# Kernel optimization log

Measured on AMD Instinct MI355X. Metric: run time of the kernel, lower is better.

Reference implementation:

```python
import jax, jax.numpy as jnp
import numpy as np

N_NODES = 50000
N_EDGES = 50000  # hyperedges
NNZ = 500000
N_GRAPHS = 50
IN_C, HID, OUT_C = 128, 256, 2


def _inv_deg(idx, num_segments):
    deg = jax.ops.segment_sum(jnp.ones(idx.shape[0], jnp.float32), idx, num_segments=num_segments)
    return jnp.where(deg > 0, 1.0 / deg, 0.0)


def hg_conv(x, W, b, rows, cols, dinv, binv):
    # PyG HypergraphConv (no attention, unit edge weights):
    # X' = D^{-1} H B^{-1} H^T (X Theta) + bias
    x = x @ W                                                    # [N, hid]
    e = jax.ops.segment_sum(x[rows], cols, num_segments=N_EDGES) * binv[:, None]   # edge feats [E, hid]
    out = jax.ops.segment_sum(e[cols], rows, num_segments=N_NODES) * dinv[:, None]  # node feats [N, hid]
    return out + b


def setup_inputs() -> dict:
    key = jax.random.key(0)
    ks = jax.random.split(key, 12)
    x = jax.random.normal(ks[0], (N_NODES, IN_C), jnp.float32)
    edge_index = jax.random.randint(ks[1], (2, NNZ), 0, N_EDGES, dtype=jnp.int64)
    batch = jnp.sort(jax.random.randint(ks[2], (N_NODES,), 0, N_GRAPHS, dtype=jnp.int64))
    s = 0.05
    return {
        "x": x, "edge_index": edge_index, "batch": batch,
        "W0": jax.random.normal(ks[3], (IN_C, HID), jnp.float32) * s,
        "b0": jnp.zeros((HID,), jnp.float32),
        "W1": jax.random.normal(ks[4], (HID, HID), jnp.float32) * s,
        "b1": jnp.zeros((HID,), jnp.float32),
        "W2": jax.random.normal(ks[5], (HID, HID), jnp.float32) * s,
        "b2": jnp.zeros((HID,), jnp.float32),
        "M1": jax.random.normal(ks[6], (HID, HID), jnp.float32) * s,
        "bM1": jnp.zeros((HID,), jnp.float32),
        "M2": jax.random.normal(ks[7], (HID, OUT_C), jnp.float32) * s,
        "bM2": jnp.zeros((OUT_C,), jnp.float32),
    }


def reference(x, edge_index, batch, W0, b0, W1, b1, W2, b2, M1, bM1, M2, bM2):
    rows, cols = edge_index[0], edge_index[1]
    dinv = _inv_deg(rows, N_NODES)   # node degree inverse
    binv = _inv_deg(cols, N_EDGES)   # hyperedge degree inverse
    h = jax.nn.relu(hg_conv(x, W0, b0, rows, cols, dinv, binv))
    h = jax.nn.relu(hg_conv(h, W1, b1, rows, cols, dinv, binv))
    h = jax.nn.relu(hg_conv(h, W2, b2, rows, cols, dinv, binv))
    # global_mean_pool (dropout is identity in eval mode)
    cnt = jax.ops.segment_sum(jnp.ones(N_NODES, jnp.float32), batch, num_segments=N_GRAPHS)
    pooled = jax.ops.segment_sum(h, batch, num_segments=N_GRAPHS) / jnp.maximum(cnt, 1.0)[:, None]
    # MLP head
    out = jax.nn.relu(pooled @ M1 + bM1) @ M2 + bM2
    return out
```

## Files before the change

kernel.cpp:

```cpp
#include <hip/hip_runtime.h>
#include <hip/hip_bf16.h>

#define NN   50000
#define NE   50000
#define NNZV 500000
#define NG   50
#define INC  128
#define HID  256
#define OUTC 2
#define STRIDE 32

typedef __bf16 bf16_t;
typedef __bf16 bf16x8 __attribute__((ext_vector_type(8)));
typedef float  f32x4  __attribute__((ext_vector_type(4)));
typedef float  f32x2  __attribute__((ext_vector_type(2)));

__device__ __forceinline__ bf16_t f2b(float f) {
  union { __hip_bfloat16 h; bf16_t b; } u;
  u.h = __float2bfloat16(f);
  return u.b;
}
__device__ __forceinline__ float b2f(bf16_t b) { return (float)b; }

template <bool HI>
__device__ __forceinline__ unsigned int fp8_pk2(float a, float b, unsigned int old) {
  return __builtin_amdgcn_cvt_pk_fp8_f32(a, b, old, HI);
}
__device__ __forceinline__ uint4 fp8_pk16(const float* v) {
  uint4 o;
  unsigned int* ow = &o.x;
#pragma unroll
  for (int wd = 0; wd < 4; wd++) {
    unsigned int u = fp8_pk2<false>(v[wd * 4 + 0], v[wd * 4 + 1], 0u);
    ow[wd] = fp8_pk2<true>(v[wd * 4 + 2], v[wd * 4 + 3], u);
  }
  return o;
}
__device__ __forceinline__ void fp8_acc16(uint4 v, f32x2* a2) {
  a2[0] += __builtin_amdgcn_cvt_pk_f32_fp8(v.x, false);
  a2[1] += __builtin_amdgcn_cvt_pk_f32_fp8(v.x, true);
  a2[2] += __builtin_amdgcn_cvt_pk_f32_fp8(v.y, false);
  a2[3] += __builtin_amdgcn_cvt_pk_f32_fp8(v.y, true);
  a2[4] += __builtin_amdgcn_cvt_pk_f32_fp8(v.z, false);
  a2[5] += __builtin_amdgcn_cvt_pk_f32_fp8(v.z, true);
  a2[6] += __builtin_amdgcn_cvt_pk_f32_fp8(v.w, false);
  a2[7] += __builtin_amdgcn_cvt_pk_f32_fp8(v.w, true);
}

__device__ __forceinline__ void wswiz_one(const float* __restrict__ W, bf16_t* __restrict__ wsw, int t) {
  int lane = t & 63;
  int nt   = (t >> 6) & 15;
  int kc   = t >> 10;
  int q = lane >> 4, n16 = lane & 15;
  bf16x8 o;
#pragma unroll
  for (int j = 0; j < 8; j++)
    o[j] = f2b(W[(size_t)(kc * 32 + q * 8 + j) * HID + nt * 16 + n16]);
  reinterpret_cast<bf16x8*>(wsw)[t] = o;
}

#define FILL_EPT   4
#define FILL_CHUNK (256 * FILL_EPT)
#define FILL_B     ((NNZV + FILL_CHUNK - 1) / FILL_CHUNK)
#define PREP_BX 1563
#define PREP_BW 80
#define PREP_BG 196

__global__ void build_kernel(const int* __restrict__ rows, const int* __restrict__ cols,
                             int* __restrict__ ncur, int* __restrict__ ecur,
                             unsigned short* __restrict__ ncol, unsigned short* __restrict__ erow,
                             const float* __restrict__ x, unsigned char* __restrict__ xb8,
                             const float* __restrict__ W0, const float* __restrict__ W1,
                             const float* __restrict__ W2, bf16_t* __restrict__ w0,
                             bf16_t* __restrict__ w1, bf16_t* __restrict__ w2,
                             const int* __restrict__ batch, int* __restrict__ gstart) {
  int blk = blockIdx.x;
  if (blk < FILL_B) {
    int base = blk * FILL_CHUNK + threadIdx.x;
#pragma unroll
    for (int e = 0; e < FILL_EPT; e++) {
      int i = base + e * 256;
      if (i < NNZV) {
        int r = rows[i], c = cols[i];
        int pe = atomicAdd(&ecur[c], 1);
        if (pe < STRIDE) erow[((size_t)c << 5) + pe] = (unsigned short)r;
        int pn = atomicAdd(&ncur[r], 1);
        if (pn < STRIDE) ncol[((size_t)r << 5) + pn] = (unsigned short)c;
      }
    }
  } else if (blk < FILL_B + PREP_BX) {
    int t = (blk - FILL_B) * 256 + threadIdx.x;
    if (t >= NN * INC / 16) return;
    const f32x4* p = reinterpret_cast<const f32x4*>(x) + (size_t)t * 4;
    float v[16];
#pragma unroll
    for (int wd = 0; wd < 4; wd++) {
      f32x4 q4 = p[wd];
#pragma unroll
      for (int j = 0; j < 4; j++) v[wd * 4 + j] = q4[j];
    }
    reinterpret_cast<uint4*>(xb8)[t] = fp8_pk16(v);
  } else if (blk < FILL_B + PREP_BX + PREP_BW) {
    int t = (blk - FILL_B - PREP_BX) * 256 + threadIdx.x;
    const int C0 = (INC / 32) * 1024;
    const int C1 = (HID / 32) * 1024;
    if (t < C0)                wswiz_one(W0, w0, t);
    else if (t < C0 + C1)      wswiz_one(W1, w1, t - C0);
    else if (t < C0 + 2 * C1)  wswiz_one(W2, w2, t - C0 - C1);
  } else {
    int i = (blk - FILL_B - PREP_BX - PREP_BW) * 256 + threadIdx.x;
    if (i >= NN) return;
    int cur  = batch[i];
    int prev = (i == 0) ? -1 : batch[i - 1];
    for (int g = prev + 1; g <= cur; g++) gstart[g] = i;
    if (i == NN - 1) {
      for (int g = cur + 1; g <= NG; g++) gstart[g] = NN;
    }
  }
}

template <int K>
__device__ __forceinline__ void gather_seg(const unsigned char* __restrict__ src,
                                           const int* __restrict__ cnt,
                                           const unsigned short* __restrict__ lst,
                                           int seg, int grp, int lr, float* acc, int& c) {
  constexpr int LPR  = K / 16;
  constexpr int NPAR = 64 / LPR;
  constexpr int MAXE = STRIDE / NPAR;
  c = min(cnt[seg], STRIDE);
  int jbeg = (c * grp) / NPAR;
  int jend = (c * (grp + 1)) / NPAR;
  int n    = jend - jbeg;
  const unsigned short* p = lst + ((size_t)seg << 5) + jbeg;
  const uint4* sv = reinterpret_cast<const uint4*>(src);
  uint4 v[MAXE];
#pragma unroll
  for (int i = 0; i < MAXE; i++) {
    if (i < n) v[i] = sv[(size_t)p[i] * LPR + lr];
  }
  f32x2* a2 = reinterpret_cast<f32x2*>(acc);
#pragma unroll
  for (int k = 0; k < 8; k++) a2[k] = f32x2{0.f, 0.f};
#pragma unroll
  for (int i = 0; i < MAXE; i++) {
    if (i < n) fp8_acc16(v[i], a2);
  }
#pragma unroll
  for (int mask = LPR; mask < 64; mask <<= 1) {
#pragma unroll
    for (int k = 0; k < 16; k++) acc[k] += __shfl_xor(acc[k], mask, 64);
  }
}

template <int W>
__global__ void seg_gather_kernel(const unsigned char* __restrict__ src,
                                  const int* __restrict__ cnt,
                                  const unsigned short* __restrict__ lst,
                                  unsigned char* __restrict__ dst, int nseg) {
  constexpr int LPR = W / 16;
  int seg  = blockIdx.x * 4 + (threadIdx.x >> 6);
  int lane = threadIdx.x & 63;
  if (seg >= nseg) return;
  int grp = lane / LPR, lr = lane % LPR;
  float acc[16];
  int c;
  gather_seg<W>(src, cnt, lst, seg, grp, lr, acc, c);
  if (grp == 0) {
    float sc = (c > 0) ? (1.0f / (float)c) : 0.f;
    float v16[16];
#pragma unroll
    for (int k = 0; k < 16; k++) v16[k] = acc[k] * sc;
    reinterpret_cast<uint4*>(dst + (size_t)seg * W + lr * 16)[0] = fp8_pk16(v16);
  }
}

template <int K, bool GRELU, bool EPI, bool OUT8>
__global__ __launch_bounds__(256) void ngemm_kernel(const unsigned char* __restrict__ src,
                                                    const int* __restrict__ cnt,
                                                    const unsigned short* __restrict__ lst,
                                                    const float* __restrict__ gbias,
                                                    const bf16_t* __restrict__ wsw,
                                                    const float* __restrict__ ebias,
                                                    void* __restrict__ Bout, int M) {
  constexpr int SW = K + 8;
  __shared__ bf16_t arows[16 * SW];
  const int tid  = threadIdx.x;
  const int wid  = tid >> 6;
  const int lane = tid & 63;
  const int mblk = blockIdx.x * 16;

  constexpr int LPR = K / 16;
  int grp = lane / LPR, lr = lane % LPR;
#pragma unroll
  for (int i = 0; i < 4; i++) {
    int row = wid * 4 + i;
    int seg = mblk + row;
    if (seg < M) {
      float acc[16];
      int c;
      gather_seg<K>(src, cnt, lst, seg, grp, lr, acc, c);
      if (grp == 0) {
        float sc = (c > 0) ? (1.0f / (float)c) : 0.f;
        bf16_t* dp = arows + row * SW + lr * 16;
        bf16x8 o0, o1;
#pragma unroll
        for (int k = 0; k < 8; k++) {
          float v0 = acc[k] * sc, v1 = acc[k + 8] * sc;
          if constexpr (GRELU) {
            v0 = fmaxf(v0 + gbias[lr * 16 + k], 0.f);
            v1 = fmaxf(v1 + gbias[lr * 16 + k + 8], 0.f);
          }
          o0[k] = f2b(v0);
          o1[k] = f2b(v1);
        }
        reinterpret_cast<bf16x8*>(dp)[0] = o0;
        reinterpret_cast<bf16x8*>(dp)[1] = o1;
      }
    }
  }
  __syncthreads();

  const int q = lane >> 4, n16 = lane & 15;
  f32x4 acc2[4];
#pragma unroll
  for (int j = 0; j < 4; j++) acc2[j] = f32x4{0.f, 0.f, 0.f, 0.f};

  const bf16x8* wv = reinterpret_cast<const bf16x8*>(wsw);
  for (int kc = 0; kc < K / 32; kc++) {
    bf16x8 af = *reinterpret_cast<const bf16x8*>(arows + n16 * SW + kc * 32 + q * 8);
    const bf16x8* wp = wv + (size_t)kc * 1024 + (size_t)(wid * 4) * 64 + lane;
#pragma unroll
    for (int j = 0; j < 4; j++) {
      bf16x8 bf = wp[j * 64];
      acc2[j] = __builtin_amdgcn_mfma_f32_16x16x32_bf16(af, bf, acc2[j], 0, 0, 0);
    }
  }

  float bcol[4];
  if constexpr (EPI) {
#pragma unroll
    for (int j = 0; j < 4; j++) bcol[j] = ebias[(wid * 4 + j) * 16 + n16];
  }

  int mb = mblk + q * 4;
#pragma unroll
  for (int r = 0; r < 4; r++) {
    int m = mb + r;
    if (m < M) {
      if constexpr (OUT8) {
        unsigned char* dst = (unsigned char*)Bout + (size_t)m * HID + n16;
#pragma unroll
        for (int j = 0; j < 4; j++) {
          float v = acc2[j][r];
          if constexpr (EPI) v = fmaxf(v + bcol[j], 0.f);
          unsigned int wbits = fp8_pk2<false>(v, v, 0u);
          dst[(wid * 4 + j) << 4] = (unsigned char)(wbits & 0xffu);
        }
      } else {
        bf16_t* dst = (bf16_t*)Bout + (size_t)m * HID + n16;
#pragma unroll
        for (int j = 0; j < 4; j++) {
          float v = acc2[j][r];
          if constexpr (EPI) v = fmaxf(v + bcol[j], 0.f);
          dst[(wid * 4 + j) << 4] = f2b(v);
        }
      }
    }
  }
}

template <int K>
__global__ __launch_bounds__(256) void ngemm2_kernel(const unsigned char* __restrict__ src,
                                                     const int* __restrict__ cnt,
                                                     const unsigned short* __restrict__ lst,
                                                     const bf16_t* __restrict__ wswA,
                                                     const float* __restrict__ biasA,
                                                     const bf16_t* __restrict__ wswB,
                                                     unsigned char* __restrict__ Bout, int M) {
  constexpr int SW  = K + 8;
  constexpr int SW2 = HID + 8;
  __shared__ bf16_t arows[16 * SW];
  __shared__ bf16_t brows[16 * SW2];
  const int tid  = threadIdx.x;
  const int wid  = tid >> 6;
  const int lane = tid & 63;
  const int mblk = blockIdx.x * 16;

  constexpr int LPR = K / 16;
  int grp = lane / LPR, lr = lane % LPR;
#pragma unroll
  for (int i = 0; i < 4; i++) {
    int row = wid * 4 + i;
    int seg = mblk + row;
    if (seg < M) {
      float acc[16];
      int c;
      gather_seg<K>(src, cnt, lst, seg, grp, lr, acc, c);
      if (grp == 0) {
        float sc = (c > 0) ? (1.0f / (float)c) : 0.f;
        bf16_t* dp = arows + row * SW + lr * 16;
        bf16x8 o0, o1;
#pragma unroll
        for (int k = 0; k < 8; k++) {
          o0[k] = f2b(acc[k] * sc);
          o1[k] = f2b(acc[k + 8] * sc);
        }
        reinterpret_cast<bf16x8*>(dp)[0] = o0;
        reinterpret_cast<bf16x8*>(dp)[1] = o1;
      }
    }
  }
  __syncthreads();

  const int q = lane >> 4, n16 = lane & 15;
  {
    f32x4 acc2[4];
#pragma unroll
    for (int j = 0; j < 4; j++) acc2[j] = f32x4{0.f, 0.f, 0.f, 0.f};
    const bf16x8* wv = reinterpret_cast<const bf16x8*>(wswA);
    for (int kc = 0; kc < K / 32; kc++) {
      bf16x8 af = *reinterpret_cast<const bf16x8*>(arows + n16 * SW + kc * 32 + q * 8);
      const bf16x8* wp = wv + (size_t)kc * 1024 + (size_t)(wid * 4) * 64 + lane;
#pragma unroll
      for (int j = 0; j < 4; j++) {
        bf16x8 bf = wp[j * 64];
        acc2[j] = __builtin_amdgcn_mfma_f32_16x16x32_bf16(af, bf, acc2[j], 0, 0, 0);
      }
    }
#pragma unroll
    for (int j = 0; j < 4; j++) {
      float bj = biasA[(wid * 4 + j) * 16 + n16];
#pragma unroll
      for (int r = 0; r < 4; r++) {
        float v = fmaxf(acc2[j][r] + bj, 0.f);
        brows[(q * 4 + r) * SW2 + (wid * 4 + j) * 16 + n16] = f2b(v);
      }
    }
  }
  __syncthreads();

  f32x4 acc3[4];
#pragma unroll
  for (int j = 0; j < 4; j++) acc3[j] = f32x4{0.f, 0.f, 0.f, 0.f};
  const bf16x8* wv = reinterpret_cast<const bf16x8*>(wswB);
  for (int kc = 0; kc < HID / 32; kc++) {
    bf16x8 af = *reinterpret_cast<const bf16x8*>(brows + n16 * SW2 + kc * 32 + q * 8);
    const bf16x8* wp = wv + (size_t)kc * 1024 + (size_t)(wid * 4) * 64 + lane;
#pragma unroll
    for (int j = 0; j < 4; j++) {
      bf16x8 bf = wp[j * 64];
      acc3[j] = __builtin_amdgcn_mfma_f32_16x16x32_bf16(af, bf, acc3[j], 0, 0, 0);
    }
  }

  int mb = mblk + q * 4;
#pragma unroll
  for (int r = 0; r < 4; r++) {
    int m = mb + r;
    if (m < M) {
      unsigned char* dst = Bout + (size_t)m * HID + n16;
#pragma unroll
      for (int j = 0; j < 4; j++) {
        float v = acc3[j][r];
        unsigned int wbits = fp8_pk2<false>(v, v, 0u);
        dst[(wid * 4 + j) << 4] = (unsigned char)(wbits & 0xffu);
      }
    }
  }
}

__global__ __launch_bounds__(256) void npool_kernel(const unsigned char* __restrict__ src,
                                                    const int* __restrict__ cnt,
                                                    const unsigned short* __restrict__ lst,
                                                    const float* __restrict__ bias,
                                                    const int* __restrict__ batch,
                                                    float* __restrict__ pooled) {
  constexpr int K = HID, SW = K + 8;
  __shared__ bf16_t arows[16 * SW];
  const int tid  = threadIdx.x;
  const int wid  = tid >> 6;
  const int lane = tid & 63;
  const int mblk = blockIdx.x * 16;

  constexpr int LPR = K / 16;
  int grp = lane / LPR, lr = lane % LPR;
#pragma unroll
  for (int i = 0; i < 4; i++) {
    int row = wid * 4 + i;
    int seg = mblk + row;
    if (seg < NN) {
      float acc[16];
      int c;
      gather_seg<K>(src, cnt, lst, seg, grp, lr, acc, c);
      if (grp == 0) {
        float sc = (c > 0) ? (1.0f / (float)c) : 0.f;
        bf16_t* dp = arows + row * SW + lr * 16;
        bf16x8 o0, o1;
#pragma unroll
        for (int k = 0; k < 8; k++) {
          o0[k] = f2b(fmaxf(acc[k] * sc + bias[lr * 16 + k], 0.f));
          o1[k] = f2b(fmaxf(acc[k + 8] * sc + bias[lr * 16 + k + 8], 0.f));
        }
        reinterpret_cast<bf16x8*>(dp)[0] = o0;
        reinterpret_cast<bf16x8*>(dp)[1] = o1;
      }
    }
  }
  __syncthreads();

  int f = tid;
  float acc = 0.f;
  int curg = -1;
  for (int r = 0; r < 16; r++) {
    int node = mblk + r;
    if (node >= NN) break;
    int g = batch[node];
    if (g != curg) {
      if (curg >= 0) atomicAdd(&pooled[(size_t)curg * HID + f], acc);
      curg = g; acc = 0.f;
    }
    acc += b2f(arows[r * SW + f]);
  }
  if (curg >= 0) atomicAdd(&pooled[(size_t)curg * HID + f], acc);
}

__global__ void head_kernel(const float* __restrict__ pooled, const int* __restrict__ gstart,
                            const float* __restrict__ M1, const float* __restrict__ bM1,
                            const float* __restrict__ M2, const float* __restrict__ bM2,
                            float* __restrict__ out) {
  int g = blockIdx.x;
  int t = threadIdx.x;
  __shared__ float p[HID];
  __shared__ float red[256];
  float cntf = (float)(gstart[g + 1] - gstart[g]);
  float inv = 1.f / fmaxf(cntf, 1.f);
  p[t] = pooled[(size_t)g * HID + t] * inv;
  __syncthreads();
  float h = bM1[t];
  for (int k = 0; k < HID; k++) h += p[k] * M1[k * HID + t];
  h = fmaxf(h, 0.f);
  float c0 = h * M2[t * OUTC + 0];
  float c1 = h * M2[t * OUTC + 1];
  red[t] = c0;
  __syncthreads();
  for (int off = 128; off > 0; off >>= 1) {
    if (t < off) red[t] += red[t + off];
    __syncthreads();
  }
  float s0 = 0.f;
  if (t == 0) s0 = red[0];
  __syncthreads();
  red[t] = c1;
  __syncthreads();
  for (int off = 128; off > 0; off >>= 1) {
    if (t < off) red[t] += red[t + off];
    __syncthreads();
  }
  if (t == 0) {
    out[g * 2 + 0] = s0 + bM2[0];
    out[g * 2 + 1] = red[0] + bM2[1];
  }
}

extern "C" void kernel_launch(void* const* d_in, const int* in_sizes, int n_in,
                              void* d_out, int out_size, void* d_ws, size_t ws_size,
                              hipStream_t stream) {
  const float* x   = (const float*)d_in[0];
  const int* ei    = (const int*)d_in[1];
  const int* rows  = ei;
  const int* cols  = ei + NNZV;
  const int* batch = (const int*)d_in[2];
  const float* W0  = (const float*)d_in[3];
  const float* b0  = (const float*)d_in[4];
  const float* W1  = (const float*)d_in[5];
  const float* b1  = (const float*)d_in[6];
  const float* W2  = (const float*)d_in[7];
  const float* b2  = (const float*)d_in[8];
  const float* M1  = (const float*)d_in[9];
  const float* bM1 = (const float*)d_in[10];
  const float* M2  = (const float*)d_in[11];
  const float* bM2 = (const float*)d_in[12];
  float* out       = (float*)d_out;

  char* w = (char*)d_ws;
  size_t off = 0;
  bf16_t* P = (bf16_t*)(w + off); off += (size_t)NN * HID * 2;
  bf16_t* Q = (bf16_t*)(w + off); off += (size_t)NE * HID * 2;
  bf16_t* R = (bf16_t*)(w + off); off += (size_t)NN * HID * 2;
  bf16_t* wsw0 = (bf16_t*)(w + off); off += (size_t)INC * HID * 2;
  bf16_t* wsw1 = (bf16_t*)(w + off); off += (size_t)HID * HID * 2;
  bf16_t* wsw2 = (bf16_t*)(w + off); off += (size_t)HID * HID * 2;
  int* gstart   = (int*)(w + off);   off += (size_t)(NG + 1) * 4;
  size_t zoff = off;
  float* pooled = (float*)(w + off); off += (size_t)NG * HID * 4;
  int* ncur     = (int*)(w + off);   off += (size_t)NN * 4;
  int* ecur     = (int*)(w + off);   off += (size_t)NE * 4;
  size_t zbytes = off - zoff;
  off = (off + 63) & ~(size_t)63;
  unsigned short* erow = (unsigned short*)(w + off); off += (size_t)NE * STRIDE * 2;
  unsigned short* ncol = (unsigned short*)(w + off); off += (size_t)NN * STRIDE * 2;

  unsigned char* xb8 = (unsigned char*)R;
  unsigned char* Qe8 = (unsigned char*)Q;
  unsigned char* Q8  = (unsigned char*)Q;
  unsigned char* P8  = (unsigned char*)P;

  (void)hipMemsetAsync(w + zoff, 0, zbytes, stream);

  const int BN = 256;
  build_kernel<<<FILL_B + PREP_BX + PREP_BW + PREP_BG, BN, 0, stream>>>(
      rows, cols, ncur, ecur, ncol, erow, x, xb8, W0, W1, W2, wsw0, wsw1, wsw2, batch, gstart);

  const int ROW_GRID16 = (NN + 15) / 16;
  const int SEG_GRID  = (NN + 3) / 4;

  seg_gather_kernel<INC><<<SEG_GRID, BN, 0, stream>>>(xb8, ecur, erow, Qe8, NE);
  ngemm2_kernel<INC><<<ROW_GRID16, BN, 0, stream>>>(Qe8, ncur, ncol, wsw0, b0, wsw1, P8, NN);
  seg_gather_kernel<HID><<<SEG_GRID, BN, 0, stream>>>(P8, ecur, erow, Q8, NE);
  ngemm_kernel<HID, true, false, true><<<ROW_GRID16, BN, 0, stream>>>(
      Q8, ncur, ncol, b1, wsw2, nullptr, P8, NN);
  seg_gather_kernel<HID><<<SEG_GRID, BN, 0, stream>>>(P8, ecur, erow, Q8, NE);
  npool_kernel<<<ROW_GRID16, BN, 0, stream>>>(Q8, ncur, ncol, b2, batch, pooled);

  head_kernel<<<NG, 256, 0, stream>>>(pooled, gstart, M1, bM1, M2, bM2, out);
}
```

Baseline: 376.4 us.

## Assign one segment per lane group and drop cross-lane shuffle reductions in gathers

The gather path changes. Instead of spreading one segment's neighbour list across every lane group of a wave and combining the partial sums with xor-shuffle reductions, each lane group now owns a whole segment and walks its list in chunks of 8. This removes the 16-way shuffle reduction and the idle lanes on the store, and packs more segments into each block. The grids are resized to match, and ngemm2 now processes 32 rows per block with two MFMA row tiles so the weight loads are reused. The fill loop is also simplified to one edge per thread. In exchange, per-lane work now depends on each segment's degree, which can cause load imbalance within a wave, and memory-level parallelism per segment is lower.

```diff
diff --git a/kernel.cpp b/kernel.cpp
--- a/kernel.cpp
+++ b/kernel.cpp
@@ -59,9 +59,7 @@
   reinterpret_cast<bf16x8*>(wsw)[t] = o;
 }
 
-#define FILL_EPT   4
-#define FILL_CHUNK (256 * FILL_EPT)
-#define FILL_B     ((NNZV + FILL_CHUNK - 1) / FILL_CHUNK)
+#define FILL_B ((NNZV + 255) / 256)
 #define PREP_BX 1563
 #define PREP_BW 80
 #define PREP_BG 196
@@ -76,17 +74,13 @@
                              const int* __restrict__ batch, int* __restrict__ gstart) {
   int blk = blockIdx.x;
   if (blk < FILL_B) {
-    int base = blk * FILL_CHUNK + threadIdx.x;
-#pragma unroll
-    for (int e = 0; e < FILL_EPT; e++) {
-      int i = base + e * 256;
-      if (i < NNZV) {
-        int r = rows[i], c = cols[i];
-        int pe = atomicAdd(&ecur[c], 1);
-        if (pe < STRIDE) erow[((size_t)c << 5) + pe] = (unsigned short)r;
-        int pn = atomicAdd(&ncur[r], 1);
-        if (pn < STRIDE) ncol[((size_t)r << 5) + pn] = (unsigned short)c;
-      }
+    int i = blk * 256 + threadIdx.x;
+    if (i < NNZV) {
+      int r = rows[i], c = cols[i];
+      int pe = atomicAdd(&ecur[c], 1);
+      int pn = atomicAdd(&ncur[r], 1);
+      if (pe < STRIDE) erow[((size_t)c << 5) + pe] = (unsigned short)r;
+      if (pn < STRIDE) ncol[((size_t)r << 5) + pn] = (unsigned short)c;
     }
   } else if (blk < FILL_B + PREP_BX) {
     int t = (blk - FILL_B) * 256 + threadIdx.x;
@@ -120,58 +114,50 @@
 }
 
 template <int K>
-__device__ __forceinline__ void gather_seg(const unsigned char* __restrict__ src,
-                                           const int* __restrict__ cnt,
-                                           const unsigned short* __restrict__ lst,
-                                           int seg, int grp, int lr, float* acc, int& c) {
-  constexpr int LPR  = K / 16;
-  constexpr int NPAR = 64 / LPR;
-  constexpr int MAXE = STRIDE / NPAR;
+__device__ __forceinline__ void gather_direct(const unsigned char* __restrict__ src,
+                                              const int* __restrict__ cnt,
+                                              const unsigned short* __restrict__ lst,
+                                              int seg, int lr, float* acc, int& c) {
+  constexpr int LPR = K / 16;
   c = min(cnt[seg], STRIDE);
-  int jbeg = (c * grp) / NPAR;
-  int jend = (c * (grp + 1)) / NPAR;
-  int n    = jend - jbeg;
-  const unsigned short* p = lst + ((size_t)seg << 5) + jbeg;
+  const unsigned short* p = lst + ((size_t)seg << 5);
   const uint4* sv = reinterpret_cast<const uint4*>(src);
-  uint4 v[MAXE];
-#pragma unroll
-  for (int i = 0; i < MAXE; i++) {
-    if (i < n) v[i] = sv[(size_t)p[i] * LPR + lr];
-  }
   f32x2* a2 = reinterpret_cast<f32x2*>(acc);
 #pragma unroll
   for (int k = 0; k < 8; k++) a2[k] = f32x2{0.f, 0.f};
-#pragma unroll
-  for (int i = 0; i < MAXE; i++) {
-    if (i < n) fp8_acc16(v[i], a2);
-  }
-#pragma unroll
-  for (int mask = LPR; mask < 64; mask <<= 1) {
-#pragma unroll
-    for (int k = 0; k < 16; k++) acc[k] += __shfl_xor(acc[k], mask, 64);
+  for (int i0 = 0; i0 < c; i0 += 8) {
+    int m = c - i0;
+    uint4 v[8];
+#pragma unroll
+    for (int j = 0; j < 8; j++)
+      if (j < m) v[j] = sv[(size_t)p[i0 + j] * LPR + lr];
+#pragma unroll
+    for (int j = 0; j < 8; j++)
+      if (j < m) fp8_acc16(v[j], a2);
   }
 }
 
 template <int W>
-__global__ void seg_gather_kernel(const unsigned char* __restrict__ src,
-                                  const int* __restrict__ cnt,
-                                  const unsigned short* __restrict__ lst,
-                                  unsigned char* __restrict__ dst, int nseg) {
+__global__ __launch_bounds__(256) void seg_gather_kernel(const unsigned char* __restrict__ src,
+                                                         const int* __restrict__ cnt,
+                                                         const unsigned short* __restrict__ lst,
+                                                         unsigned char* __restrict__ dst, int nseg) {
   constexpr int LPR = W / 16;
-  int seg  = blockIdx.x * 4 + (threadIdx.x >> 6);
-  int lane = threadIdx.x & 63;
+  constexpr int SPW = 64 / LPR;
+  constexpr int SPB = 4 * SPW;
+  const int lane = threadIdx.x & 63;
+  const int wid  = threadIdx.x >> 6;
+  const int sub  = lane / LPR, lr = lane % LPR;
+  int seg = blockIdx.x * SPB + wid * SPW + sub;
   if (seg >= nseg) return;
-  int grp = lane / LPR, lr = lane % LPR;
   float acc[16];
   int c;
-  gather_seg<W>(src, cnt, lst, seg, grp, lr, acc, c);
-  if (grp == 0) {
-    float sc = (c > 0) ? (1.0f / (float)c) : 0.f;
-    float v16[16];
-#pragma unroll
-    for (int k = 0; k < 16; k++) v16[k] = acc[k] * sc;
-    reinterpret_cast<uint4*>(dst + (size_t)seg * W + lr * 16)[0] = fp8_pk16(v16);
-  }
+  gather_direct<W>(src, cnt, lst, seg, lr, acc, c);
+  float sc = (c > 0) ? (1.0f / (float)c) : 0.f;
+  float v16[16];
+#pragma unroll
+  for (int k = 0; k < 16; k++) v16[k] = acc[k] * sc;
+  reinterpret_cast<uint4*>(dst + (size_t)seg * W + lr * 16)[0] = fp8_pk16(v16);
 }
 
 template <int K, bool GRELU, bool EPI, bool OUT8>
@@ -190,32 +176,30 @@
   const int mblk = blockIdx.x * 16;
 
   constexpr int LPR = K / 16;
-  int grp = lane / LPR, lr = lane % LPR;
-#pragma unroll
-  for (int i = 0; i < 4; i++) {
-    int row = wid * 4 + i;
+  constexpr int SPW = 64 / LPR;
+  const int sub = lane / LPR, lr = lane % LPR;
+  {
+    int row = wid * SPW + sub;
     int seg = mblk + row;
     if (seg < M) {
       float acc[16];
       int c;
-      gather_seg<K>(src, cnt, lst, seg, grp, lr, acc, c);
-      if (grp == 0) {
-        float sc = (c > 0) ? (1.0f / (float)c) : 0.f;
-        bf16_t* dp = arows + row * SW + lr * 16;
-        bf16x8 o0, o1;
-#pragma unroll
-        for (int k = 0; k < 8; k++) {
-          float v0 = acc[k] * sc, v1 = acc[k + 8] * sc;
-          if constexpr (GRELU) {
-            v0 = fmaxf(v0 + gbias[lr * 16 + k], 0.f);
-            v1 = fmaxf(v1 + gbias[lr * 16 + k + 8], 0.f);
-          }
-          o0[k] = f2b(v0);
-          o1[k] = f2b(v1);
+      gather_direct<K>(src, cnt, lst, seg, lr, acc, c);
+      float sc = (c > 0) ? (1.0f / (float)c) : 0.f;
+      bf16_t* dp = arows + row * SW + lr * 16;
+      bf16x8 o0, o1;
+#pragma unroll
+      for (int k = 0; k < 8; k++) {
+        float v0 = acc[k] * sc, v1 = acc[k + 8] * sc;
+        if constexpr (GRELU) {
+          v0 = fmaxf(v0 + gbias[lr * 16 + k], 0.f);
+          v1 = fmaxf(v1 + gbias[lr * 16 + k + 8], 0.f);
         }
-        reinterpret_cast<bf16x8*>(dp)[0] = o0;
-        reinterpret_cast<bf16x8*>(dp)[1] = o1;
-      }
+        o0[k] = f2b(v0);
+        o1[k] = f2b(v1);
+      }
+      reinterpret_cast<bf16x8*>(dp)[0] = o0;
+      reinterpret_cast<bf16x8*>(dp)[1] = o1;
     }
   }
   __syncthreads();
@@ -279,91 +263,103 @@
                                                      unsigned char* __restrict__ Bout, int M) {
   constexpr int SW  = K + 8;
   constexpr int SW2 = HID + 8;
-  __shared__ bf16_t arows[16 * SW];
-  __shared__ bf16_t brows[16 * SW2];
+  constexpr int LPR = K / 16;
+  constexpr int SPW = 64 / LPR;
+  __shared__ bf16_t arows[32 * SW];
+  __shared__ bf16_t brows[32 * SW2];
   const int tid  = threadIdx.x;
   const int wid  = tid >> 6;
   const int lane = tid & 63;
-  const int mblk = blockIdx.x * 16;
-
-  constexpr int LPR = K / 16;
-  int grp = lane / LPR, lr = lane % LPR;
-#pragma unroll
-  for (int i = 0; i < 4; i++) {
-    int row = wid * 4 + i;
+  const int mblk = blockIdx.x * 32;
+
+  {
+    const int sub = lane / LPR, lr = lane % LPR;
+    int row = wid * SPW + sub;
     int seg = mblk + row;
     if (seg < M) {
       float acc[16];
       int c;
-      gather_seg<K>(src, cnt, lst, seg, grp, lr, acc, c);
-      if (grp == 0) {
-        float sc = (c > 0) ? (1.0f / (float)c) : 0.f;
-        bf16_t* dp = arows + row * SW + lr * 16;
-        bf16x8 o0, o1;
-#pragma unroll
-        for (int k = 0; k < 8; k++) {
-          o0[k] = f2b(acc[k] * sc);
-          o1[k] = f2b(acc[k + 8] * sc);
-        }
-        reinterpret_cast<bf16x8*>(dp)[0] = o0;
-        reinterpret_cast<bf16x8*>(dp)[1] = o1;
-      }
+      gather_direct<K>(src, cnt, lst, seg, lr, acc, c);
+      float sc = (c > 0) ? (1.0f / (float)c) : 0.f;
+      bf16_t* dp = arows + row * SW + lr * 16;
+      bf16x8 o0, o1;
+#pragma unroll
+      for (int k = 0; k < 8; k++) {
+        o0[k] = f2b(acc[k] * sc);
+        o1[k] = f2b(acc[k + 8] * sc);
+      }
+      reinterpret_cast<bf16x8*>(dp)[0] = o0;
+      reinterpret_cast<bf16x8*>(dp)[1] = o1;
     }
   }
   __syncthreads();
 
   const int q = lane >> 4, n16 = lane & 15;
   {
-    f32x4 acc2[4];
-#pragma unroll
-    for (int j = 0; j < 4; j++) acc2[j] = f32x4{0.f, 0.f, 0.f, 0.f};
+    f32x4 acc2[2][4];
+#pragma unroll
+    for (int a = 0; a < 2; a++)
+#pragma unroll
+      for (int j = 0; j < 4; j++) acc2[a][j] = f32x4{0.f, 0.f, 0.f, 0.f};
     const bf16x8* wv = reinterpret_cast<const bf16x8*>(wswA);
     for (int kc = 0; kc < K / 32; kc++) {
-      bf16x8 af = *reinterpret_cast<const bf16x8*>(arows + n16 * SW + kc * 32 + q * 8);
+      bf16x8 af0 = *reinterpret_cast<const bf16x8*>(arows + n16 * SW + kc * 32 + q * 8);
+      bf16x8 af1 = *reinterpret_cast<const bf16x8*>(arows + (n16 + 16) * SW + kc * 32 + q * 8);
       const bf16x8* wp = wv + (size_t)kc * 1024 + (size_t)(wid * 4) * 64 + lane;
 #pragma unroll
       for (int j = 0; j < 4; j++) {
         bf16x8 bf = wp[j * 64];
-        acc2[j] = __builtin_amdgcn_mfma_f32_16x16x32_bf16(af, bf, acc2[j], 0, 0, 0);
-      }
-    }
-#pragma unroll
-    for (int j = 0; j < 4; j++) {
-      float bj = biasA[(wid * 4 + j) * 16 + n16];
-#pragma unroll
-      for (int r = 0; r < 4; r++) {
-        float v = fmaxf(acc2[j][r] + bj, 0.f);
-        brows[(q * 4 + r) * SW2 + (wid * 4 + j) * 16 + n16] = f2b(v);
-      }
-    }
-  }
-  __syncthreads();
-
-  f32x4 acc3[4];
-#pragma unroll
-  for (int j = 0; j < 4; j++) acc3[j] = f32x4{0.f, 0.f, 0.f, 0.f};
+        acc2[0][j] = __builtin_amdgcn_mfma_f32_16x16x32_bf16(af0, bf, acc2[0][j], 0, 0, 0);
+        acc2[1][j] = __builtin_amdgcn_mfma_f32_16x16x32_bf16(af1, bf, acc2[1][j], 0, 0, 0);
+      }
+    }
+#pragma unroll
+    for (int a = 0; a < 2; a++) {
+#pragma unroll
+      for (int j = 0; j < 4; j++) {
+        float bj = biasA[(wid * 4 + j) * 16 + n16];
+#pragma unroll
+        for (int r = 0; r < 4; r++) {
+          float v = fmaxf(acc2[a][j][r] + bj, 0.f);
+          brows[(a * 16 + q * 4 + r) * SW2 + (wid * 4 + j) * 16 + n16] = f2b(v);
+        }
+      }
+    }
+  }
+  __syncthreads();
+
+  f32x4 acc3[2][4];
+#pragma unroll
+  for (int a = 0; a < 2; a++)
+#pragma unroll
+    for (int j = 0; j < 4; j++) acc3[a][j] = f32x4{0.f, 0.f, 0.f, 0.f};
   const bf16x8* wv = reinterpret_cast<const bf16x8*>(wswB);
   for (int kc = 0; kc < HID / 32; kc++) {
-    bf16x8 af = *reinterpret_cast<const bf16x8*>(brows + n16 * SW2 + kc * 32 + q * 8);
+    bf16x8 af0 = *reinterpret_cast<const bf16x8*>(brows + n16 * SW2 + kc * 32 + q * 8);
+    bf16x8 af1 = *reinterpret_cast<const bf16x8*>(brows + (n16 + 16) * SW2 + kc * 32 + q * 8);
     const bf16x8* wp = wv + (size_t)kc * 1024 + (size_t)(wid * 4) * 64 + lane;
 #pragma unroll
     for (int j = 0; j < 4; j++) {
       bf16x8 bf = wp[j * 64];
-      acc3[j] = __builtin_amdgcn_mfma_f32_16x16x32_bf16(af, bf, acc3[j], 0, 0, 0);
-    }
-  }
-
-  int mb = mblk + q * 4;
-#pragma unroll
-  for (int r = 0; r < 4; r++) {
-    int m = mb + r;
-    if (m < M) {
-      unsigned char* dst = Bout + (size_t)m * HID + n16;
-#pragma unroll
-      for (int j = 0; j < 4; j++) {
-        float v = acc3[j][r];
-        unsigned int wbits = fp8_pk2<false>(v, v, 0u);
-        dst[(wid * 4 + j) << 4] = (unsigned char)(wbits & 0xffu);
+      acc3[0][j] = __builtin_amdgcn_mfma_f32_16x16x32_bf16(af0, bf, acc3[0][j], 0, 0, 0);
+      acc3[1][j] = __builtin_amdgcn_mfma_f32_16x16x32_bf16(af1, bf, acc3[1][j], 0, 0, 0);
+    }
+  }
+
+#pragma unroll
+  for (int a = 0; a < 2; a++) {
+    int mb = mblk + a * 16 + q * 4;
+#pragma unroll
+    for (int r = 0; r < 4; r++) {
+      int m = mb + r;
+      if (m < M) {
+        unsigned char* dst = Bout + (size_t)m * HID + n16;
+#pragma unroll
+        for (int j = 0; j < 4; j++) {
+          float v = acc3[a][j][r];
+          unsigned int wbits = fp8_pk2<false>(v, v, 0u);
+          dst[(wid * 4 + j) << 4] = (unsigned char)(wbits & 0xffu);
+        }
       }
     }
   }
@@ -383,27 +379,25 @@
   const int mblk = blockIdx.x * 16;
 
   constexpr int LPR = K / 16;
-  int grp = lane / LPR, lr = lane % LPR;
-#pragma unroll
-  for (int i = 0; i < 4; i++) {
-    int row = wid * 4 + i;
+  constexpr int SPW = 64 / LPR;
+  const int sub = lane / LPR, lr = lane % LPR;
+  {
+    int row = wid * SPW + sub;
     int seg = mblk + row;
     if (seg < NN) {
       float acc[16];
       int c;
-      gather_seg<K>(src, cnt, lst, seg, grp, lr, acc, c);
-      if (grp == 0) {
-        float sc = (c > 0) ? (1.0f / (float)c) : 0.f;
-        bf16_t* dp = arows + row * SW + lr * 16;
-        bf16x8 o0, o1;
-#pragma unroll
-        for (int k = 0; k < 8; k++) {
-          o0[k] = f2b(fmaxf(acc[k] * sc + bias[lr * 16 + k], 0.f));
-          o1[k] = f2b(fmaxf(acc[k + 8] * sc + bias[lr * 16 + k + 8], 0.f));
-        }
-        reinterpret_cast<bf16x8*>(dp)[0] = o0;
-        reinterpret_cast<bf16x8*>(dp)[1] = o1;
-      }
+      gather_direct<K>(src, cnt, lst, seg, lr, acc, c);
+      float sc = (c > 0) ? (1.0f / (float)c) : 0.f;
+      bf16_t* dp = arows + row * SW + lr * 16;
+      bf16x8 o0, o1;
+#pragma unroll
+      for (int k = 0; k < 8; k++) {
+        o0[k] = f2b(fmaxf(acc[k] * sc + bias[lr * 16 + k], 0.f));
+        o1[k] = f2b(fmaxf(acc[k + 8] * sc + bias[lr * 16 + k + 8], 0.f));
+      }
+      reinterpret_cast<bf16x8*>(dp)[0] = o0;
+      reinterpret_cast<bf16x8*>(dp)[1] = o1;
     }
   }
   __syncthreads();
@@ -511,16 +505,13 @@
   build_kernel<<<FILL_B + PREP_BX + PREP_BW + PREP_BG, BN, 0, stream>>>(
       rows, cols, ncur, ecur, ncol, erow, x, xb8, W0, W1, W2, wsw0, wsw1, wsw2, batch, gstart);
 
-  const int ROW_GRID16 = (NN + 15) / 16;
-  const int SEG_GRID  = (NN + 3) / 4;
-
-  seg_gather_kernel<INC><<<SEG_GRID, BN, 0, stream>>>(xb8, ecur, erow, Qe8, NE);
-  ngemm2_kernel<INC><<<ROW_GRID16, BN, 0, stream>>>(Qe8, ncur, ncol, wsw0, b0, wsw1, P8, NN);
-  seg_gather_kernel<HID><<<SEG_GRID, BN, 0, stream>>>(P8, ecur, erow, Q8, NE);
-  ngemm_kernel<HID, true, false, true><<<ROW_GRID16, BN, 0, stream>>>(
+  seg_gather_kernel<INC><<<(NE + 31) / 32, BN, 0, stream>>>(xb8, ecur, erow, Qe8, NE);
+  ngemm2_kernel<INC><<<(NN + 31) / 32, BN, 0, stream>>>(Qe8, ncur, ncol, wsw0, b0, wsw1, P8, NN);
+  seg_gather_kernel<HID><<<(NE + 15) / 16, BN, 0, stream>>>(P8, ecur, erow, Q8, NE);
+  ngemm_kernel<HID, true, false, true><<<(NN + 15) / 16, BN, 0, stream>>>(
       Q8, ncur, ncol, b1, wsw2, nullptr, P8, NN);
-  seg_gather_kernel<HID><<<SEG_GRID, BN, 0, stream>>>(P8, ecur, erow, Q8, NE);
-  npool_kernel<<<ROW_GRID16, BN, 0, stream>>>(Q8, ncur, ncol, b2, batch, pooled);
+  seg_gather_kernel<HID><<<(NE + 15) / 16, BN, 0, stream>>>(P8, ecur, erow, Q8, NE);
+  npool_kernel<<<(NN + 15) / 16, BN, 0, stream>>>(Q8, ncur, ncol, b2, batch, pooled);
 
   head_kernel<<<NG, 256, 0, stream>>>(pooled, gstart, M1, bM1, M2, bM2, out);
 }
```

Result: faster. 364.2 us (-3.2%).
